# Performance work log

Hardware: AMD Instinct MI355X
Metric: run time of the kernel (lower is better)

## Reference

```python
import jax, jax.numpy as jnp
import numpy as np

B, T, F, H = 8, 1024, 1024, 16
DK = F // H


def setup_inputs() -> dict:
    key = jax.random.key(0)
    ks = jax.random.split(key, 12)
    s = 1.0 / np.sqrt(F)
    return {
        "query": jax.random.normal(ks[0], (B, T, F), jnp.float32),
        "key": jax.random.normal(ks[1], (B, T, F), jnp.float32),
        "value": jax.random.normal(ks[2], (B, T, F), jnp.float32),
        "mask": jnp.ones((B, T), jnp.float32),
        "Wq": jax.random.normal(ks[3], (F, F), jnp.float32) * s,
        "bq": jax.random.normal(ks[4], (F,), jnp.float32) * s,
        "Wk": jax.random.normal(ks[5], (F, F), jnp.float32) * s,
        "bk": jax.random.normal(ks[6], (F,), jnp.float32) * s,
        "Wv": jax.random.normal(ks[7], (F, F), jnp.float32) * s,
        "bv": jax.random.normal(ks[8], (F,), jnp.float32) * s,
        "Wo": jax.random.normal(ks[9], (F, F), jnp.float32) * s,
        "bo": jax.random.normal(ks[10], (F,), jnp.float32) * s,
    }


def reference(query, key, value, mask, Wq, bq, Wk, bk, Wv, bv, Wo, bo):
    # projections, split into heads: (B, H, T, DK)
    def proj(x, W, b):
        y = x @ W.T + b
        return y.reshape(B, -1, H, DK).transpose(0, 2, 1, 3)

    q = proj(query, Wq, bq)
    k = proj(key, Wk, bk)
    v = proj(value, Wv, bv)

    scores = jnp.einsum("bhqd,bhkd->bhqk", q, k) / jnp.sqrt(jnp.float32(DK))
    attn = jax.nn.softmax(scores, axis=-1)  # dropout is identity (eval / p=0)
    x = jnp.einsum("bhqk,bhkd->bhqd", attn, v)
    x = x.transpose(0, 2, 1, 3).reshape(B, -1, F)
    x = x @ Wo.T + bo
    return x * mask[..., None]
```

## Files before the change

kernel.cpp:

```cpp
#include <hip/hip_runtime.h>
#include <hip/hip_bf16.h>

typedef unsigned short u16;
typedef unsigned int u32;
typedef __attribute__((ext_vector_type(8))) short bf16x8;
typedef __attribute__((ext_vector_type(8))) unsigned short u16x8;
typedef __attribute__((ext_vector_type(4))) unsigned short u16x4;
typedef __attribute__((ext_vector_type(4))) float f32x4;

#define DEVI __device__ __forceinline__

static constexpr int Bn = 8, Tn = 1024, Fn = 1024, Hn = 16, DKn = 64;
static constexpr int Mtot = Bn * Tn;

DEVI u16 f2bf(float x) {
  unsigned u = __builtin_bit_cast(unsigned, x);
  u += 0x7fffu + ((u >> 16) & 1u);
  return (u16)(u >> 16);
}

DEVI u32 cvt_pk_bf16(float lo, float hi) {
  u32 r;
  asm("v_cvt_pk_bf16_f32 %0, %1, %2" : "=v"(r) : "v"(lo), "v"(hi));
  return r;
}

DEVI float fast_exp2(float x) { return __builtin_amdgcn_exp2f(x); }

DEVI f32x4 mfma16(bf16x8 a, bf16x8 b, f32x4 c) {
  return __builtin_amdgcn_mfma_f32_16x16x32_bf16(a, b, c, 0, 0, 0);
}

typedef const __attribute__((address_space(1))) void GAS;
typedef __attribute__((address_space(3))) void LAS;
#define GLL16(gp, lp) __builtin_amdgcn_global_load_lds((GAS*)(gp), (LAS*)(lp), 16, 0, 0)

DEVI void cvt_chunk(const float* __restrict__ in, u16* __restrict__ out, int i) {
  const float4* p = reinterpret_cast<const float4*>(in + i);
  float4 a = p[0], b = p[1];
  float v[8] = {a.x, a.y, a.z, a.w, b.x, b.y, b.z, b.w};
  u16x8 r;
#pragma unroll
  for (int j = 0; j < 8; j++) r[j] = f2bf(v[j]);
  *reinterpret_cast<u16x8*>(out + i) = r;
}

__global__ __launch_bounds__(256) void cvt4(const float* __restrict__ a, const float* __restrict__ b,
                                            const float* __restrict__ c, const float* __restrict__ e,
                                            u16* __restrict__ oa, u16* __restrict__ ob,
                                            u16* __restrict__ oc, u16* __restrict__ oe) {
  const int id = blockIdx.x * 256 + threadIdx.x;
  const int seg = id >> 17;
  const int off = (id & 131071) * 8;
  const float* s = seg == 0 ? a : (seg == 1 ? b : (seg == 2 ? c : e));
  u16* d = seg == 0 ? oa : (seg == 1 ? ob : (seg == 2 ? oc : oe));
  cvt_chunk(s, d, off);
}

__global__ __launch_bounds__(256, 1) void gemm_qk(
    const float* __restrict__ Aq, const float* __restrict__ Ak,
    const u16* __restrict__ Wqb, const u16* __restrict__ Wkb,
    const float* __restrict__ bq, const float* __restrict__ bk,
    u16* __restrict__ Qo, u16* __restrict__ Ko, float SC) {
  constexpr int Kd = 1024;
  __shared__ u16 sA[2][128 * 64];
  __shared__ u16 sB[2][128 * 64];
  const int tid = threadIdx.x;
  const int l = tid & 63, w = tid >> 6;
  const int wm = w >> 1, wn = w & 1;
  const int lr = l & 15, g = l >> 4;
  const int p = blockIdx.y;
  const float* A = p == 0 ? Aq : Ak;
  const u16* Bw = p == 0 ? Wqb : Wkb;
  const float* bias = p == 0 ? bq : bk;
  u16* Obf = p == 0 ? Qo : Ko;
  const float oscale = p == 0 ? SC : 1.0f;
  const int bid = blockIdx.x;
  const int wg = (bid & 7) * 64 + (bid >> 3);
  const int m0 = (wg >> 3) * 128, n0 = (wg & 7) * 128;

  f32x4 acc[4][4];
#pragma unroll
  for (int i = 0; i < 4; i++)
#pragma unroll
    for (int j = 0; j < 4; j++) acc[i][j] = f32x4{0.f, 0.f, 0.f, 0.f};

  int aoffF[4], awb[4];
#pragma unroll
  for (int i = 0; i < 4; i++) {
    const int c = i * 256 + tid;
    const int r = c >> 3, cc = c & 7;
    aoffF[i] = r * Kd + cc * 8;
    awb[i] = r * 128 + ((cc ^ (r & 7)) << 4);
  }
  int boff[4];
#pragma unroll
  for (int i = 0; i < 4; i++) {
    const int c = i * 256 + tid;
    const int r = c >> 3, cc = (c & 7) ^ (r & 7);
    boff[i] = r * Kd + cc * 8;
  }
  const float* Af = A + (size_t)m0 * Kd;
  const u16* Bbase = Bw + (size_t)n0 * Kd;

  float4 ra[4][2];
  auto loadA = [&](int kt) {
#pragma unroll
    for (int i = 0; i < 4; i++) {
      const float* s = Af + kt * 64 + aoffF[i];
      ra[i][0] = *reinterpret_cast<const float4*>(s);
      ra[i][1] = *reinterpret_cast<const float4*>(s + 4);
    }
  };
  auto writeA = [&](int buf) {
#pragma unroll
    for (int i = 0; i < 4; i++) {
      uint4 pk;
      pk.x = cvt_pk_bf16(ra[i][0].x, ra[i][0].y);
      pk.y = cvt_pk_bf16(ra[i][0].z, ra[i][0].w);
      pk.z = cvt_pk_bf16(ra[i][1].x, ra[i][1].y);
      pk.w = cvt_pk_bf16(ra[i][1].z, ra[i][1].w);
      *reinterpret_cast<uint4*>((char*)&sA[buf][0] + awb[i]) = pk;
    }
  };
  auto stageB = [&](int buf, int kt) {
#pragma unroll
    for (int i = 0; i < 4; i++)
      GLL16(Bbase + kt * 64 + boff[i], (char*)&sB[buf][0] + (i * 256 + w * 64) * 16);
  };

  loadA(0);
  stageB(0, 0);
  writeA(0);
  for (int t = 0; t < 16; ++t) {
    const int cur = t & 1;
    if (t < 15) {
      loadA(t + 1);
      stageB(cur ^ 1, t + 1);
      asm volatile("s_waitcnt vmcnt(12) lgkmcnt(0)" ::: "memory");
    } else {
      asm volatile("s_waitcnt vmcnt(0) lgkmcnt(0)" ::: "memory");
    }
    asm volatile("s_barrier" ::: "memory");
#pragma unroll
    for (int ks = 0; ks < 2; ks++) {
      bf16x8 af[4], bfr[4];
#pragma unroll
      for (int mi = 0; mi < 4; mi++) {
        const int row = wm * 64 + mi * 16 + lr;
        af[mi] = *reinterpret_cast<const bf16x8*>(
            (const char*)&sA[cur][0] + row * 128 + ((ks * 64 + g * 16) ^ ((row & 7) << 4)));
      }
#pragma unroll
      for (int ni = 0; ni < 4; ni++) {
        const int row = wn * 64 + ni * 16 + lr;
        bfr[ni] = *reinterpret_cast<const bf16x8*>(
            (const char*)&sB[cur][0] + row * 128 + ((ks * 64 + g * 16) ^ ((row & 7) << 4)));
      }
      __builtin_amdgcn_s_setprio(1);
#pragma unroll
      for (int mi = 0; mi < 4; mi++)
#pragma unroll
        for (int ni = 0; ni < 4; ni++) acc[ni][mi] = mfma16(bfr[ni], af[mi], acc[ni][mi]);
      __builtin_amdgcn_s_setprio(0);
    }
    if (t < 15) writeA(cur ^ 1);
    asm volatile("s_barrier" ::: "memory");
  }

#pragma unroll
  for (int ni = 0; ni < 4; ni++) {
    const int nb = n0 + wn * 64 + ni * 16 + g * 4;
    const float4 b4 = *reinterpret_cast<const float4*>(&bias[nb]);
#pragma unroll
    for (int mi = 0; mi < 4; mi++) {
      const int m = m0 + wm * 64 + mi * 16 + lr;
      const f32x4 a = acc[ni][mi];
      const int b = m >> 10, tt = m & 1023;
      const int h = nb >> 6, dk0 = nb & 63;
      u16x4 pk;
      pk[0] = f2bf((a[0] + b4.x) * oscale);
      pk[1] = f2bf((a[1] + b4.y) * oscale);
      pk[2] = f2bf((a[2] + b4.z) * oscale);
      pk[3] = f2bf((a[3] + b4.w) * oscale);
      *reinterpret_cast<u16x4*>(&Obf[((((size_t)b * 16 + h) * 1024 + tt) * 64) + dk0]) = pk;
    }
  }
}

__global__ __launch_bounds__(256, 1) void gemm_v(const float* __restrict__ A,
                                                 const u16* __restrict__ Bw,
                                                 const float* __restrict__ bias,
                                                 u16* __restrict__ Obf) {
  constexpr int Kd = 1024;
  __shared__ u16 sA[2][128 * 64];
  __shared__ u16 sB[2][128 * 64];
  const int tid = threadIdx.x;
  const int l = tid & 63, w = tid >> 6;
  const int wm = w >> 1, wn = w & 1;
  const int lr = l & 15, g = l >> 4;
  const int bid = blockIdx.x;
  const int wg = (bid & 7) * 64 + (bid >> 3);
  const int m0 = (wg >> 3) * 128, n0 = (wg & 7) * 128;

  f32x4 acc[4][4];
#pragma unroll
  for (int i = 0; i < 4; i++)
#pragma unroll
    for (int j = 0; j < 4; j++) acc[i][j] = f32x4{0.f, 0.f, 0.f, 0.f};

  int aoffF[4], awb[4];
#pragma unroll
  for (int i = 0; i < 4; i++) {
    const int c = i * 256 + tid;
    const int r = c >> 3, cc = c & 7;
    aoffF[i] = r * Kd + cc * 8;
    awb[i] = r * 128 + ((cc ^ (r & 7)) << 4);
  }
  int boff[4];
#pragma unroll
  for (int i = 0; i < 4; i++) {
    const int c = i * 256 + tid;
    const int r = c >> 3, cc = (c & 7) ^ (r & 7);
    boff[i] = r * Kd + cc * 8;
  }
  const float* Af = A + (size_t)m0 * Kd;
  const u16* Bbase = Bw + (size_t)n0 * Kd;

  float4 ra[4][2];
  auto loadA = [&](int kt) {
#pragma unroll
    for (int i = 0; i < 4; i++) {
      const float* s = Af + kt * 64 + aoffF[i];
      ra[i][0] = *reinterpret_cast<const float4*>(s);
      ra[i][1] = *reinterpret_cast<const float4*>(s + 4);
    }
  };
  auto writeA = [&](int buf) {
#pragma unroll
    for (int i = 0; i < 4; i++) {
      uint4 pk;
      pk.x = cvt_pk_bf16(ra[i][0].x, ra[i][0].y);
      pk.y = cvt_pk_bf16(ra[i][0].z, ra[i][0].w);
      pk.z = cvt_pk_bf16(ra[i][1].x, ra[i][1].y);
      pk.w = cvt_pk_bf16(ra[i][1].z, ra[i][1].w);
      *reinterpret_cast<uint4*>((char*)&sA[buf][0] + awb[i]) = pk;
    }
  };
  auto stageB = [&](int buf, int kt) {
#pragma unroll
    for (int i = 0; i < 4; i++)
      GLL16(Bbase + kt * 64 + boff[i], (char*)&sB[buf][0] + (i * 256 + w * 64) * 16);
  };

  loadA(0);
  stageB(0, 0);
  writeA(0);
  for (int t = 0; t < 16; ++t) {
    const int cur = t & 1;
    if (t < 15) {
      loadA(t + 1);
      stageB(cur ^ 1, t + 1);
      asm volatile("s_waitcnt vmcnt(12) lgkmcnt(0)" ::: "memory");
    } else {
      asm volatile("s_waitcnt vmcnt(0) lgkmcnt(0)" ::: "memory");
    }
    asm volatile("s_barrier" ::: "memory");
#pragma unroll
    for (int ks = 0; ks < 2; ks++) {
      bf16x8 af[4], bfr[4];
#pragma unroll
      for (int mi = 0; mi < 4; mi++) {
        const int row = wm * 64 + mi * 16 + lr;
        af[mi] = *reinterpret_cast<const bf16x8*>(
            (const char*)&sA[cur][0] + row * 128 + ((ks * 64 + g * 16) ^ ((row & 7) << 4)));
      }
#pragma unroll
      for (int ni = 0; ni < 4; ni++) {
        const int row = wn * 64 + ni * 16 + lr;
        bfr[ni] = *reinterpret_cast<const bf16x8*>(
            (const char*)&sB[cur][0] + row * 128 + ((ks * 64 + g * 16) ^ ((row & 7) << 4)));
      }
      __builtin_amdgcn_s_setprio(1);
#pragma unroll
      for (int mi = 0; mi < 4; mi++)
#pragma unroll
        for (int ni = 0; ni < 4; ni++) acc[mi][ni] = mfma16(af[mi], bfr[ni], acc[mi][ni]);
      __builtin_amdgcn_s_setprio(0);
    }
    if (t < 15) writeA(cur ^ 1);
    asm volatile("s_barrier" ::: "memory");
  }

#pragma unroll
  for (int ni = 0; ni < 4; ni++) {
    const int n = n0 + wn * 64 + ni * 16 + lr;
    const float bv = bias[n];
    const int h = n >> 6, dk = n & 63;
#pragma unroll
    for (int mi = 0; mi < 4; mi++) {
      const int mb = m0 + wm * 64 + mi * 16 + g * 4;
      u16x4 pk;
#pragma unroll
      for (int j = 0; j < 4; j++) pk[j] = f2bf(acc[mi][ni][j] + bv);
      const int b = mb >> 10, tt = mb & 1023;
      size_t idx = (((size_t)b * 16 + h) * 64 + dk) * 1024 + tt;
      *reinterpret_cast<u16x4*>(Obf + idx) = pk;
    }
  }
}

__global__ __launch_bounds__(256, 1) void gemm_out(const u16* __restrict__ A,
                                                   const u16* __restrict__ Bw,
                                                   const float* __restrict__ bias,
                                                   const float* __restrict__ mask,
                                                   float* __restrict__ Of) {
  constexpr int Kd = 1024;
  __shared__ u16 sA[2][128 * 64];
  __shared__ u16 sB[2][128 * 64];
  const int tid = threadIdx.x;
  const int l = tid & 63, w = tid >> 6;
  const int wm = w >> 1, wn = w & 1;
  const int lr = l & 15, g = l >> 4;
  const int bid = blockIdx.x;
  const int wg = (bid & 7) * 64 + (bid >> 3);
  const int m0 = (wg >> 3) * 128, n0 = (wg & 7) * 128;

  f32x4 acc[4][4];
#pragma unroll
  for (int i = 0; i < 4; i++)
#pragma unroll
    for (int j = 0; j < 4; j++) acc[i][j] = f32x4{0.f, 0.f, 0.f, 0.f};

  int aoff[4], boff[4];
#pragma unroll
  for (int i = 0; i < 4; i++) {
    const int c = i * 256 + tid;
    const int r = c >> 3, cc = (c & 7) ^ (r & 7);
    aoff[i] = r * Kd + cc * 8;
    boff[i] = r * Kd + cc * 8;
  }
  const u16* Abase = A + (size_t)m0 * Kd;
  const u16* Bbase = Bw + (size_t)n0 * Kd;

  auto stage = [&](int buf, int kt) {
#pragma unroll
    for (int i = 0; i < 4; i++)
      GLL16(Abase + kt * 64 + aoff[i], (char*)&sA[buf][0] + (i * 256 + w * 64) * 16);
#pragma unroll
    for (int i = 0; i < 4; i++)
      GLL16(Bbase + kt * 64 + boff[i], (char*)&sB[buf][0] + (i * 256 + w * 64) * 16);
  };

  stage(0, 0);
  for (int t = 0; t < 16; ++t) {
    const int cur = t & 1;
    if (t < 15) {
      stage(cur ^ 1, t + 1);
      asm volatile("s_waitcnt vmcnt(8)" ::: "memory");
    } else {
      asm volatile("s_waitcnt vmcnt(0)" ::: "memory");
    }
    asm volatile("s_barrier" ::: "memory");
#pragma unroll
    for (int ks = 0; ks < 2; ks++) {
      bf16x8 af[4], bfr[4];
#pragma unroll
      for (int mi = 0; mi < 4; mi++) {
        const int row = wm * 64 + mi * 16 + lr;
        af[mi] = *reinterpret_cast<const bf16x8*>(
            (const char*)&sA[cur][0] + row * 128 + ((ks * 64 + g * 16) ^ ((row & 7) << 4)));
      }
#pragma unroll
      for (int ni = 0; ni < 4; ni++) {
        const int row = wn * 64 + ni * 16 + lr;
        bfr[ni] = *reinterpret_cast<const bf16x8*>(
            (const char*)&sB[cur][0] + row * 128 + ((ks * 64 + g * 16) ^ ((row & 7) << 4)));
      }
      __builtin_amdgcn_s_setprio(1);
#pragma unroll
      for (int mi = 0; mi < 4; mi++)
#pragma unroll
        for (int ni = 0; ni < 4; ni++) acc[ni][mi] = mfma16(bfr[ni], af[mi], acc[ni][mi]);
      __builtin_amdgcn_s_setprio(0);
    }
    asm volatile("s_barrier" ::: "memory");
  }

#pragma unroll
  for (int ni = 0; ni < 4; ni++) {
    const int nb = n0 + wn * 64 + ni * 16 + g * 4;
    const float4 b4 = *reinterpret_cast<const float4*>(&bias[nb]);
#pragma unroll
    for (int mi = 0; mi < 4; mi++) {
      const int m = m0 + wm * 64 + mi * 16 + lr;
      const f32x4 a = acc[ni][mi];
      const float mk = mask[m];
      float4 o;
      o.x = (a[0] + b4.x) * mk;
      o.y = (a[1] + b4.y) * mk;
      o.z = (a[2] + b4.z) * mk;
      o.w = (a[3] + b4.w) * mk;
      *reinterpret_cast<float4*>(&Of[(size_t)m * 1024 + nb]) = o;
    }
  }
}

__global__ __launch_bounds__(512, 1) void flash_attn(const u16* __restrict__ Qb,
                                                     const u16* __restrict__ Kb,
                                                     const u16* __restrict__ Vt,
                                                     u16* __restrict__ ctx) {
  __shared__ u16 sK[2][64 * 64];
  __shared__ u16 sV[64 * 64];
  __shared__ u16 pbuf[8][16 * 64];
  const int tid = threadIdx.x, l = tid & 63, w = tid >> 6;
  const int lr = l & 15, g = l >> 4;
  const int wg = ((blockIdx.x & 7) << 6) + (blockIdx.x >> 3);
  const int qt = wg & 3, bh = wg >> 2;
  const u16* Qh = Qb + (size_t)bh * (Tn * DKn);
  const u16* Kh = Kb + (size_t)bh * (Tn * DKn);
  const u16* Vh = Vt + (size_t)bh * (Tn * DKn);

  bf16x8 aq[2][2];
  int qrow[2];
#pragma unroll
  for (int qg = 0; qg < 2; qg++) {
    qrow[qg] = qt * 256 + w * 32 + qg * 16 + lr;
    aq[qg][0] = *reinterpret_cast<const bf16x8*>(Qh + (size_t)qrow[qg] * 64 + g * 8);
    aq[qg][1] = *reinterpret_cast<const bf16x8*>(Qh + (size_t)qrow[qg] * 64 + 32 + g * 8);
  }

  float mrow[2] = {-1e30f, -1e30f}, lsum[2] = {0.f, 0.f};
  f32x4 of[2][4];
#pragma unroll
  for (int qg = 0; qg < 2; qg++)
#pragma unroll
    for (int c = 0; c < 4; c++) of[qg][c] = f32x4{0.f, 0.f, 0.f, 0.f};

  char* pb = (char*)&pbuf[w][0];
  const int sw = (lr & 7) << 4;
  int wadr[4];
#pragma unroll
  for (int c = 0; c < 4; c++) wadr[c] = lr * 128 + (((c * 16 + g * 4) * 2) ^ sw);
  const int radr0 = lr * 128 + ((g * 16) ^ sw);
  const int radr1 = lr * 128 + ((64 + g * 16) ^ sw);

  const int sr = tid >> 3;
  const int sc = (tid & 7) ^ (sr & 7);
  auto stageK = [&](int buf, int kv0) {
    GLL16((const char*)Kh + ((size_t)(kv0 + sr) << 7) + (sc << 4),
          (char*)&sK[buf][0] + w * 1024);
  };
  auto stageV = [&](int kv0) {
    GLL16((const char*)Vh + ((size_t)sr << 11) + kv0 * 2 + (sc << 4),
          (char*)&sV[0] + w * 1024);
  };

  stageK(0, 0);
  stageV(0);
  __syncthreads();
  int cur = 0;

  for (int t = 0; t < 16; t++) {
    if (t < 15) stageK(cur ^ 1, (t + 1) * 64);
    const char* kb = (const char*)&sK[cur][0];
    const char* vb = (const char*)&sV[0];

    f32x4 sf[2][4];
    __builtin_amdgcn_s_setprio(1);
#pragma unroll
    for (int c = 0; c < 4; c++) {
      const char* kr = kb + (c * 16 + lr) * 128;
      bf16x8 k0 = *reinterpret_cast<const bf16x8*>(kr + ((g * 16) ^ sw));
      bf16x8 k1 = *reinterpret_cast<const bf16x8*>(kr + ((64 + g * 16) ^ sw));
      f32x4 z0 = mfma16(k0, aq[0][0], f32x4{0.f, 0.f, 0.f, 0.f});
      sf[0][c] = mfma16(k1, aq[0][1], z0);
      f32x4 z1 = mfma16(k0, aq[1][0], f32x4{0.f, 0.f, 0.f, 0.f});
      sf[1][c] = mfma16(k1, aq[1][1], z1);
    }
    __builtin_amdgcn_s_setprio(0);

    bf16x8 ap[2][2];
#pragma unroll
    for (int qg = 0; qg < 2; qg++) {
      f32x4 mx4 = sf[qg][0];
#pragma unroll
      for (int c = 1; c < 4; c++)
#pragma unroll
        for (int j = 0; j < 4; j++) mx4[j] = fmaxf(mx4[j], sf[qg][c][j]);
      const float pmax = fmaxf(fmaxf(mx4[0], mx4[1]), fmaxf(mx4[2], mx4[3]));
      if (__any(pmax > mrow[qg] + 8.0f)) {
        float mx = pmax;
        mx = fmaxf(mx, __shfl_xor(mx, 16));
        mx = fmaxf(mx, __shfl_xor(mx, 32));
        const float mn = fmaxf(mrow[qg], mx);
        const float alpha = fast_exp2(mrow[qg] - mn);
        mrow[qg] = mn;
        lsum[qg] *= alpha;
#pragma unroll
        for (int c = 0; c < 4; c++)
#pragma unroll
          for (int j = 0; j < 4; j++) of[qg][c][j] *= alpha;
      }
      const float mn = mrow[qg];
      float rs = 0.f;
#pragma unroll
      for (int c = 0; c < 4; c++)
#pragma unroll
        for (int j = 0; j < 4; j++) {
          float pp = fast_exp2(sf[qg][c][j] - mn);
          sf[qg][c][j] = pp;
          rs += pp;
        }
      lsum[qg] += rs;

#pragma unroll
      for (int c = 0; c < 4; c++) {
        uint2 pk;
        pk.x = cvt_pk_bf16(sf[qg][c][0], sf[qg][c][1]);
        pk.y = cvt_pk_bf16(sf[qg][c][2], sf[qg][c][3]);
        *reinterpret_cast<uint2*>(pb + wadr[c]) = pk;
      }
      ap[qg][0] = *reinterpret_cast<const bf16x8*>(pb + radr0);
      ap[qg][1] = *reinterpret_cast<const bf16x8*>(pb + radr1);
    }

    __syncthreads();

    __builtin_amdgcn_s_setprio(1);
#pragma unroll
    for (int d0 = 0; d0 < 4; d0++) {
      const char* vr = vb + (d0 * 16 + lr) * 128;
      bf16x8 v0 = *reinterpret_cast<const bf16x8*>(vr + ((g * 16) ^ sw));
      bf16x8 v1 = *reinterpret_cast<const bf16x8*>(vr + ((64 + g * 16) ^ sw));
#pragma unroll
      for (int qg = 0; qg < 2; qg++) {
        f32x4 z = mfma16(v0, ap[qg][0], of[qg][d0]);
        of[qg][d0] = mfma16(v1, ap[qg][1], z);
      }
    }
    __builtin_amdgcn_s_setprio(0);

    __syncthreads();
    if (t < 15) stageV((t + 1) * 64);
    cur ^= 1;
  }

  const int b = bh >> 4, h = bh & 15;
#pragma unroll
  for (int qg = 0; qg < 2; qg++) {
    float ls = lsum[qg];
    ls += __shfl_xor(ls, 16);
    ls += __shfl_xor(ls, 32);
    const float inv = 1.0f / ls;
    const size_t base = ((size_t)b * 1024 + qrow[qg]) * 1024 + h * 64;
#pragma unroll
    for (int d0 = 0; d0 < 4; d0++) {
      uint2 pk;
      pk.x = cvt_pk_bf16(of[qg][d0][0] * inv, of[qg][d0][1] * inv);
      pk.y = cvt_pk_bf16(of[qg][d0][2] * inv, of[qg][d0][3] * inv);
      *reinterpret_cast<uint2*>(ctx + base + d0 * 16 + g * 4) = pk;
    }
  }
}

extern "C" void kernel_launch(void* const* d_in, const int* in_sizes, int n_in,
                              void* d_out, int out_size, void* d_ws, size_t ws_size,
                              hipStream_t stream) {
  const float* query = (const float*)d_in[0];
  const float* key = (const float*)d_in[1];
  const float* value = (const float*)d_in[2];
  const float* mask = (const float*)d_in[3];
  const float* Wq = (const float*)d_in[4];
  const float* bq = (const float*)d_in[5];
  const float* Wk = (const float*)d_in[6];
  const float* bk = (const float*)d_in[7];
  const float* Wv = (const float*)d_in[8];
  const float* bv = (const float*)d_in[9];
  const float* Wo = (const float*)d_in[10];
  const float* bo = (const float*)d_in[11];
  (void)in_sizes; (void)n_in; (void)out_size; (void)ws_size;

  u16* ws = (u16*)d_ws;
  const size_t MB8 = (size_t)8 << 20;
  u16* ctx = ws;
  u16* Wqb = ws + 3 * MB8;
  u16* Wkb = Wqb + (1 << 20);
  u16* Wvb = Wkb + (1 << 20);
  u16* Wob = Wvb + (1 << 20);
  u16* Qb = Wob + (1 << 20);
  u16* Kb = Qb + MB8;
  u16* Vtb = Kb + MB8;

  cvt4<<<2048, 256, 0, stream>>>(Wq, Wk, Wv, Wo, Wqb, Wkb, Wvb, Wob);

  const float SC = 0.125f * 1.44269504089f;
  const int ng = (Mtot / 128) * (Fn / 128);
  gemm_qk<<<dim3(ng, 2), 256, 0, stream>>>(query, key, Wqb, Wkb, bq, bk, Qb, Kb, SC);
  gemm_v<<<ng, 256, 0, stream>>>(value, Wvb, bv, Vtb);

  flash_attn<<<Bn * Hn * (Tn / 256), 512, 0, stream>>>(Qb, Kb, Vtb, ctx);

  gemm_out<<<ng, 256, 0, stream>>>(ctx, Wob, bo, mask, (float*)d_out);
}
```

Baseline: 170.5 us.

## Widen flash-attention KV tile to 128 and process query groups sequentially

The attention kernel now stages 128 keys/values per iteration instead of 64, which halves the loop trip count and the number of block barriers. It also restructures each iteration so the two 16-row query groups are handled one after another, each doing QK, softmax and PV in turn, instead of computing all scores first. Together these are meant to cut synchronisation overhead and register pressure per group. In exchange the kernel uses twice the shared memory and issues more LDS reads per tile, with a barrier placed inside the query-group loop.

```diff
diff --git a/kernel.cpp b/kernel.cpp
--- a/kernel.cpp
+++ b/kernel.cpp
@@ -410,9 +410,9 @@
                                                      const u16* __restrict__ Kb,
                                                      const u16* __restrict__ Vt,
                                                      u16* __restrict__ ctx) {
-  __shared__ u16 sK[2][64 * 64];
-  __shared__ u16 sV[64 * 64];
-  __shared__ u16 pbuf[8][16 * 64];
+  __shared__ u16 sK[2][128 * 64];
+  __shared__ u16 sV[64 * 128];
+  __shared__ u16 pbuf[8][16 * 128];
   const int tid = threadIdx.x, l = tid & 63, w = tid >> 6;
   const int lr = l & 15, g = l >> 4;
   const int wg = ((blockIdx.x & 7) << 6) + (blockIdx.x >> 3);
@@ -439,21 +439,32 @@
 
   char* pb = (char*)&pbuf[w][0];
   const int sw = (lr & 7) << 4;
-  int wadr[4];
-#pragma unroll
-  for (int c = 0; c < 4; c++) wadr[c] = lr * 128 + (((c * 16 + g * 4) * 2) ^ sw);
-  const int radr0 = lr * 128 + ((g * 16) ^ sw);
-  const int radr1 = lr * 128 + ((64 + g * 16) ^ sw);
-
-  const int sr = tid >> 3;
-  const int sc = (tid & 7) ^ (sr & 7);
+  int wadr[8];
+#pragma unroll
+  for (int c = 0; c < 8; c++) wadr[c] = lr * 256 + (((c * 16 + g * 4) * 2) ^ sw);
+  int radr[4];
+#pragma unroll
+  for (int s = 0; s < 4; s++) radr[s] = lr * 256 + ((s * 64 + g * 16) ^ sw);
+
   auto stageK = [&](int buf, int kv0) {
-    GLL16((const char*)Kh + ((size_t)(kv0 + sr) << 7) + (sc << 4),
-          (char*)&sK[buf][0] + w * 1024);
+#pragma unroll
+    for (int i = 0; i < 2; i++) {
+      const int c2 = i * 512 + tid;
+      const int r = c2 >> 3, cc = c2 & 7;
+      const int sc = cc ^ (r & 7);
+      GLL16((const char*)Kh + ((size_t)(kv0 + r) << 7) + (sc << 4),
+            (char*)&sK[buf][0] + i * 8192 + w * 1024);
+    }
   };
   auto stageV = [&](int kv0) {
-    GLL16((const char*)Vh + ((size_t)sr << 11) + kv0 * 2 + (sc << 4),
-          (char*)&sV[0] + w * 1024);
+#pragma unroll
+    for (int i = 0; i < 2; i++) {
+      const int c2 = i * 512 + tid;
+      const int r = c2 >> 4, cc = c2 & 15;
+      const int sc = (cc & 8) | ((cc & 7) ^ (r & 7));
+      GLL16((const char*)Vh + ((size_t)r << 11) + kv0 * 2 + (sc << 4),
+            (char*)&sV[0] + i * 8192 + w * 1024);
+    }
   };
 
   stageK(0, 0);
@@ -461,33 +472,32 @@
   __syncthreads();
   int cur = 0;
 
-  for (int t = 0; t < 16; t++) {
-    if (t < 15) stageK(cur ^ 1, (t + 1) * 64);
+  for (int t = 0; t < 8; t++) {
+    if (t < 7) stageK(cur ^ 1, (t + 1) * 128);
     const char* kb = (const char*)&sK[cur][0];
     const char* vb = (const char*)&sV[0];
 
-    f32x4 sf[2][4];
-    __builtin_amdgcn_s_setprio(1);
-#pragma unroll
-    for (int c = 0; c < 4; c++) {
-      const char* kr = kb + (c * 16 + lr) * 128;
-      bf16x8 k0 = *reinterpret_cast<const bf16x8*>(kr + ((g * 16) ^ sw));
-      bf16x8 k1 = *reinterpret_cast<const bf16x8*>(kr + ((64 + g * 16) ^ sw));
-      f32x4 z0 = mfma16(k0, aq[0][0], f32x4{0.f, 0.f, 0.f, 0.f});
-      sf[0][c] = mfma16(k1, aq[0][1], z0);
-      f32x4 z1 = mfma16(k0, aq[1][0], f32x4{0.f, 0.f, 0.f, 0.f});
-      sf[1][c] = mfma16(k1, aq[1][1], z1);
-    }
-    __builtin_amdgcn_s_setprio(0);
-
-    bf16x8 ap[2][2];
 #pragma unroll
     for (int qg = 0; qg < 2; qg++) {
-      f32x4 mx4 = sf[qg][0];
-#pragma unroll
-      for (int c = 1; c < 4; c++)
-#pragma unroll
-        for (int j = 0; j < 4; j++) mx4[j] = fmaxf(mx4[j], sf[qg][c][j]);
+      f32x4 sf[8];
+      __builtin_amdgcn_s_setprio(1);
+#pragma unroll
+      for (int c = 0; c < 8; c++) {
+        const char* kr = kb + (c * 16 + lr) * 128;
+        bf16x8 k0 = *reinterpret_cast<const bf16x8*>(kr + ((g * 16) ^ sw));
+        bf16x8 k1 = *reinterpret_cast<const bf16x8*>(kr + ((64 + g * 16) ^ sw));
+        f32x4 z = mfma16(k0, aq[qg][0], f32x4{0.f, 0.f, 0.f, 0.f});
+        sf[c] = mfma16(k1, aq[qg][1], z);
+      }
+      __builtin_amdgcn_s_setprio(0);
+
+      if (qg == 0) __syncthreads();
+
+      f32x4 mx4 = sf[0];
+#pragma unroll
+      for (int c = 1; c < 8; c++)
+#pragma unroll
+        for (int j = 0; j < 4; j++) mx4[j] = fmaxf(mx4[j], sf[c][j]);
       const float pmax = fmaxf(fmaxf(mx4[0], mx4[1]), fmaxf(mx4[2], mx4[3]));
       if (__any(pmax > mrow[qg] + 8.0f)) {
         float mx = pmax;
@@ -505,44 +515,39 @@
       const float mn = mrow[qg];
       float rs = 0.f;
 #pragma unroll
-      for (int c = 0; c < 4; c++)
+      for (int c = 0; c < 8; c++)
 #pragma unroll
         for (int j = 0; j < 4; j++) {
-          float pp = fast_exp2(sf[qg][c][j] - mn);
-          sf[qg][c][j] = pp;
+          float pp = fast_exp2(sf[c][j] - mn);
+          sf[c][j] = pp;
           rs += pp;
         }
       lsum[qg] += rs;
 
 #pragma unroll
-      for (int c = 0; c < 4; c++) {
+      for (int c = 0; c < 8; c++) {
         uint2 pk;
-        pk.x = cvt_pk_bf16(sf[qg][c][0], sf[qg][c][1]);
-        pk.y = cvt_pk_bf16(sf[qg][c][2], sf[qg][c][3]);
+        pk.x = cvt_pk_bf16(sf[c][0], sf[c][1]);
+        pk.y = cvt_pk_bf16(sf[c][2], sf[c][3]);
         *reinterpret_cast<uint2*>(pb + wadr[c]) = pk;
       }
-      ap[qg][0] = *reinterpret_cast<const bf16x8*>(pb + radr0);
-      ap[qg][1] = *reinterpret_cast<const bf16x8*>(pb + radr1);
+
+      __builtin_amdgcn_s_setprio(1);
+#pragma unroll
+      for (int s = 0; s < 4; s++) {
+        const bf16x8 ap = *reinterpret_cast<const bf16x8*>(pb + radr[s]);
+#pragma unroll
+        for (int d0 = 0; d0 < 4; d0++) {
+          const char* vr = vb + (d0 * 16 + lr) * 256;
+          bf16x8 v = *reinterpret_cast<const bf16x8*>(vr + ((s * 64 + g * 16) ^ sw));
+          of[qg][d0] = mfma16(v, ap, of[qg][d0]);
+        }
+      }
+      __builtin_amdgcn_s_setprio(0);
     }
 
     __syncthreads();
-
-    __builtin_amdgcn_s_setprio(1);
-#pragma unroll
-    for (int d0 = 0; d0 < 4; d0++) {
-      const char* vr = vb + (d0 * 16 + lr) * 128;
-      bf16x8 v0 = *reinterpret_cast<const bf16x8*>(vr + ((g * 16) ^ sw));
-      bf16x8 v1 = *reinterpret_cast<const bf16x8*>(vr + ((64 + g * 16) ^ sw));
-#pragma unroll
-      for (int qg = 0; qg < 2; qg++) {
-        f32x4 z = mfma16(v0, ap[qg][0], of[qg][d0]);
-        of[qg][d0] = mfma16(v1, ap[qg][1], z);
-      }
-    }
-    __builtin_amdgcn_s_setprio(0);
-
-    __syncthreads();
-    if (t < 15) stageV((t + 1) * 64);
+    if (t < 7) stageV((t + 1) * 128);
     cur ^= 1;
   }
 
```

Measured after the change: 183.5 us. 7.6% more time.
